# Optimization experiments

Hardware: AMD Instinct MI355X
Metric: run time of the kernel (lower is better)

## Reference

```python
import jax, jax.numpy as jnp
import numpy as np

NODE_DIM = 128
DEPTH = 4
N_NODES = 10000
N_EDGES = 320000


def setup_inputs() -> dict:
    key = jax.random.key(0)
    ks = jax.random.split(key, 12)
    s = 0.05
    D = NODE_DIM
    inp = {
        'h': jax.random.normal(ks[0], (N_NODES, D), jnp.float32),
        'x': jax.random.normal(ks[1], (N_NODES, 3), jnp.float32),
        'edges': jax.random.randint(ks[2], (2, N_EDGES), 0, N_NODES, jnp.int32),
        # edge_mlp: Linear(2D+1 -> D), SiLU, Linear(D -> D), SiLU  (per layer)
        'edge_w1': jax.random.normal(ks[3], (DEPTH, 2 * D + 1, D), jnp.float32) * s,
        'edge_b1': jnp.zeros((DEPTH, D), jnp.float32),
        'edge_w2': jax.random.normal(ks[4], (DEPTH, D, D), jnp.float32) * s,
        'edge_b2': jnp.zeros((DEPTH, D), jnp.float32),
        # node_mlp: Linear(2D -> D), SiLU, Linear(D -> D)  (per layer)
        'node_w1': jax.random.normal(ks[5], (DEPTH, 2 * D, D), jnp.float32) * s,
        'node_b1': jnp.zeros((DEPTH, D), jnp.float32),
        'node_w2': jax.random.normal(ks[6], (DEPTH, D, D), jnp.float32) * s,
        'node_b2': jnp.zeros((DEPTH, D), jnp.float32),
        # coord_mlp (only used by last layer, update_coords=True):
        # Linear(D -> D), SiLU, Linear(D -> 1, bias=False)
        'coord_w1': jax.random.normal(ks[7], (D, D), jnp.float32) * s,
        'coord_b1': jnp.zeros((D,), jnp.float32),
        'coord_w2': jax.random.normal(ks[8], (D, 1), jnp.float32) * s,
    }
    return inp


def reference(h, x, edges, edge_w1, edge_b1, edge_w2, edge_b2,
              node_w1, node_b1, node_w2, node_b2,
              coord_w1, coord_b1, coord_w2):
    silu = jax.nn.silu
    row, col = edges[0], edges[1]
    n = h.shape[0]
    for i in range(DEPTH):
        # coord2radial
        coord_diff = x[row] - x[col]                       # [E, 3]
        radial = jnp.sum(coord_diff * coord_diff, axis=-1, keepdims=True)  # [E, 1]
        # edge_model: m_ij = edge_mlp([h_i, h_j, radial])
        feat = jnp.concatenate([h[row], h[col], radial], axis=-1)  # [E, 2D+1]
        m = silu(feat @ edge_w1[i] + edge_b1[i])
        m = silu(m @ edge_w2[i] + edge_b2[i])              # [E, D]
        # coord_model (only last layer, coords_agg='mean')
        if i == DEPTH - 1:
            w = silu(m @ coord_w1 + coord_b1) @ coord_w2   # [E, 1]
            trans = coord_diff * w                          # [E, 3]
            agg = jax.ops.segment_sum(trans, row, num_segments=n)
            cnt = jax.ops.segment_sum(jnp.ones((row.shape[0], 1), trans.dtype),
                                      row, num_segments=n)
            x = x + agg / jnp.maximum(cnt, 1.0)
        # node_model: h = h + node_mlp([h, sum_j m_ij])  (residual=True)
        magg = jax.ops.segment_sum(m, row, num_segments=n)  # [N, D]
        hin = jnp.concatenate([h, magg], axis=-1)           # [N, 2D]
        out = silu(hin @ node_w1[i] + node_b1[i]) @ node_w2[i] + node_b2[i]
        h = h + out
    return h, x
```

## Files before the change

### kernel.cpp

```cpp
#include <hip/hip_runtime.h>

#define NND 10000
#define NE  320000
#define DD  128
#define NDEPTH 4
#define TE  64

typedef __attribute__((ext_vector_type(8))) short s8b;
typedef __attribute__((ext_vector_type(4))) float f4;
typedef unsigned short u16;
typedef unsigned int   u32;

__device__ __forceinline__ u16 f2b(float f) {
    u32 u = __builtin_bit_cast(u32, f);
    u32 r = (u + 0x7fffu + ((u >> 16) & 1u)) >> 16;
    return (u16)r;
}

__device__ __forceinline__ float b2f(u16 b) {
    u32 u = (u32)b << 16;
    return __builtin_bit_cast(float, u);
}

__device__ __forceinline__ void bpair(u32 v, float& lo, float& hi) {
    lo = __builtin_bit_cast(float, v << 16);
    hi = __builtin_bit_cast(float, v & 0xffff0000u);
}

__device__ __forceinline__ u32 cvt_pk(float lo, float hi) {
    u32 r;
    asm("v_cvt_pk_bf16_f32 %0, %1, %2" : "=v"(r) : "v"(lo), "v"(hi));
    return r;
}

__device__ __forceinline__ u16 f2b1(float v) {
    return (u16)cvt_pk(v, v);
}

__device__ __forceinline__ float silu_f(float v) {
    return v * __builtin_amdgcn_rcpf(1.0f + __expf(-v));
}

__device__ __forceinline__ s8b frag_a(const u16* rowp, int g) {
    union { s8b v; uint2 u2[2]; } r;
    r.u2[0] = *(const uint2*)(rowp + 4 * g);
    r.u2[1] = *(const uint2*)(rowp + 16 + 4 * g);
    return r.v;
}

__device__ __forceinline__ f4 mfma16(s8b a, s8b b, f4 c) {
    return __builtin_amdgcn_mfma_f32_16x16x32_bf16(a, b, c, 0, 0, 0);
}

__global__ __launch_bounds__(256) void egnn_pack(
    const float* __restrict__ ew1, const float* __restrict__ ew2,
    const float* __restrict__ nw1, const float* __restrict__ nw2,
    const float* __restrict__ cw1, u16* __restrict__ pw)
{
    int t = blockIdx.x * 256 + threadIdx.x;
    if (t >= 25 * 16384) return;
    int mat = t >> 14;
    int r   = t & 16383;
    int kt  = r >> 12;
    int nt  = (r >> 9) & 7;
    int lane= (r >> 3) & 63;
    int j   = r & 7;
    int g = lane >> 4, l15 = lane & 15;
    int k = kt * 32 + ((j < 4) ? (4 * g + j) : (16 + 4 * g + (j - 4)));
    int n = nt * 16 + l15;
    float v;
    if (mat < 24) {
        int layer = mat / 6, tp = mat % 6;
        switch (tp) {
            case 0: v = ew1[((size_t)layer * 257 + k) * DD + n]; break;
            case 1: v = ew1[((size_t)layer * 257 + 128 + k) * DD + n]; break;
            case 2: v = ew2[((size_t)layer * 128 + k) * DD + n]; break;
            case 3: v = nw1[((size_t)layer * 256 + k) * DD + n]; break;
            case 4: v = nw1[((size_t)layer * 256 + 128 + k) * DD + n]; break;
            default: v = nw2[((size_t)layer * 128 + k) * DD + n]; break;
        }
    } else {
        v = cw1[(size_t)k * DD + n];
    }
    pw[t] = f2b(v);
}

__global__ __launch_bounds__(256) void egnn_init(
    const float* __restrict__ h, u16* __restrict__ hb)
{
    int i = blockIdx.x * 256 + threadIdx.x;
    size_t base = (size_t)i * 4;
    if (base >= (size_t)NND * DD) return;
    float4 v = *(const float4*)(h + base);
    union { u16 s[4]; uint2 u; } t2;
    t2.s[0] = f2b(v.x); t2.s[1] = f2b(v.y); t2.s[2] = f2b(v.z); t2.s[3] = f2b(v.w);
    *(uint2*)(hb + base) = t2.u;
}

__global__ __launch_bounds__(256) void egnn_count(
    const int* __restrict__ edges, int* __restrict__ cnts)
{
    int e = blockIdx.x * 256 + threadIdx.x;
    if (e < NE) atomicAdd(&cnts[edges[e]], 1);
}

__global__ __launch_bounds__(1024) void egnn_scan(
    const int* __restrict__ cnts, int* __restrict__ off, int* __restrict__ cursor)
{
    __shared__ int part[1024];
    const int t = threadIdx.x;
    const int base = t * 10;
    int s = 0;
    #pragma unroll
    for (int j = 0; j < 10; ++j) {
        int i = base + j;
        s += (i < NND) ? cnts[i] : 0;
    }
    part[t] = s;
    __syncthreads();
    for (int d = 1; d < 1024; d <<= 1) {
        int v = (t >= d) ? part[t - d] : 0;
        __syncthreads();
        part[t] += v;
        __syncthreads();
    }
    int run = (t == 0) ? 0 : part[t - 1];
    #pragma unroll
    for (int j = 0; j < 10; ++j) {
        int i = base + j;
        if (i <= NND) { off[i] = run; cursor[i] = run; }
        if (i < NND) run += cnts[i];
    }
}

__global__ __launch_bounds__(256) void egnn_scatter(
    const int* __restrict__ edges, int* __restrict__ cursor,
    int* __restrict__ rows, int* __restrict__ cols)
{
    int e = blockIdx.x * 256 + threadIdx.x;
    if (e >= NE) return;
    int r = edges[e];
    int p = atomicAdd(&cursor[r], 1);
    rows[p] = r;
    cols[p] = edges[NE + e];
}

__global__ __launch_bounds__(256) void egnn_pre0(
    const u16* __restrict__ hb, const u16* __restrict__ pw,
    const float* __restrict__ eb1,
    float* __restrict__ Pb, u16* __restrict__ Qb)
{
    __shared__ __attribute__((aligned(16))) u16 tH[64][136];
    const int tid = threadIdx.x;
    const int n0  = blockIdx.x * 64;

    #pragma unroll
    for (int it = 0; it < 4; ++it) {
        int idx = tid + it * 256;
        int el = idx >> 4, part = idx & 15;
        int node = n0 + el;
        if (node < NND) {
            *(uint4*)&tH[el][part * 8] = *(const uint4*)(hb + (size_t)node * DD + part * 8);
        } else {
            uint4 z = {0u, 0u, 0u, 0u};
            *(uint4*)&tH[el][part * 8] = z;
        }
    }
    __syncthreads();

    const int wv = tid >> 6, lane = tid & 63;
    const int g = lane >> 4, l15 = lane & 15;
    const int wrow = wv * 16;

    f4 accP[8], accQ[8];
    #pragma unroll
    for (int nt = 0; nt < 8; ++nt) { accP[nt] = f4{0.f,0.f,0.f,0.f}; accQ[nt] = f4{0.f,0.f,0.f,0.f}; }
    const u16* pwa = pw;
    const u16* pwb = pw + 16384;
    #pragma unroll
    for (int kt = 0; kt < 4; ++kt) {
        s8b a = frag_a(&tH[wrow + l15][kt * 32], g);
        const u16* ba = pwa + (size_t)kt * 4096 + lane * 8;
        const u16* bb = pwb + (size_t)kt * 4096 + lane * 8;
        #pragma unroll
        for (int nt = 0; nt < 8; ++nt) {
            accP[nt] = mfma16(a, *(const s8b*)(ba + nt * 512), accP[nt]);
            accQ[nt] = mfma16(a, *(const s8b*)(bb + nt * 512), accQ[nt]);
        }
    }
    #pragma unroll
    for (int nt = 0; nt < 8; ++nt) {
        int n = nt * 16 + l15;
        float bb = eb1[n];
        #pragma unroll
        for (int r = 0; r < 4; ++r) {
            int node = n0 + wrow + g * 4 + r;
            if (node < NND) {
                Pb[(size_t)node * DD + n] = accP[nt][r] + bb;
                Qb[(size_t)node * DD + n] = f2b1(accQ[nt][r]);
            }
        }
    }
}

__global__ __launch_bounds__(256, 6) void egnn_edge(
    const float* __restrict__ Pb, const u16* __restrict__ Qb,
    const float* __restrict__ xin,
    const int* __restrict__ rows, const int* __restrict__ cols,
    const u16* __restrict__ pw,
    const float* __restrict__ ew1,
    const float* __restrict__ eb2, const float* __restrict__ cb1,
    const float* __restrict__ cw2,
    float* __restrict__ magg, float* __restrict__ aggx,
    int layer, int last)
{
    __shared__ __attribute__((aligned(16))) u16 tA[TE][136];
    __shared__ float rad[TE];
    __shared__ float cdf[TE][3];
    __shared__ int   ridx[TE];
    __shared__ int   cidx[TE];
    __shared__ unsigned char segflag[TE + 1];

    const int tid = threadIdx.x;
    const int nblk = NE / TE;
    const int bid  = blockIdx.x;
    const int blk  = (bid & 7) * (nblk >> 3) + (bid >> 3);
    const int p0   = blk * TE;

    if (tid < TE) {
        int p = p0 + tid;
        int r = rows[p];
        int c = cols[p];
        ridx[tid] = r; cidx[tid] = c;
        float d0 = xin[r * 3 + 0] - xin[c * 3 + 0];
        float d1 = xin[r * 3 + 1] - xin[c * 3 + 1];
        float d2 = xin[r * 3 + 2] - xin[c * 3 + 2];
        rad[tid] = d0 * d0 + d1 * d1 + d2 * d2;
        cdf[tid][0] = d0; cdf[tid][1] = d1; cdf[tid][2] = d2;
    }
    __syncthreads();

    if (tid < TE) {
        segflag[tid] = (tid == 0) || (ridx[tid] != ridx[tid - 1]);
        if (tid == 0) segflag[TE] = 1;
    }

    {
        const int cg = tid & 15;
        const int rg = tid >> 4;
        const float* wrp = ew1 + ((size_t)layer * 257 + 256) * DD + cg * 8;
        float4 w0 = *(const float4*)(wrp);
        float4 w4 = *(const float4*)(wrp + 4);
        #pragma unroll
        for (int k = 0; k < 4; ++k) {
            int row = rg + 16 * k;
            int rn = ridx[row], cn = cidx[row];
            float rd = rad[row];
            const float* pp = Pb + (size_t)rn * DD + cg * 8;
            float4 pa = *(const float4*)(pp);
            float4 pc = *(const float4*)(pp + 4);
            uint4 qv = *(const uint4*)(Qb + (size_t)cn * DD + cg * 8);
            float q0, q1, q2, q3, q4, q5, q6, q7;
            bpair(qv.x, q0, q1);
            bpair(qv.y, q2, q3);
            bpair(qv.z, q4, q5);
            bpair(qv.w, q6, q7);
            float v0 = silu_f(pa.x + q0 + rd * w0.x);
            float v1 = silu_f(pa.y + q1 + rd * w0.y);
            float v2 = silu_f(pa.z + q2 + rd * w0.z);
            float v3 = silu_f(pa.w + q3 + rd * w0.w);
            float v4 = silu_f(pc.x + q4 + rd * w4.x);
            float v5 = silu_f(pc.y + q5 + rd * w4.y);
            float v6 = silu_f(pc.z + q6 + rd * w4.z);
            float v7 = silu_f(pc.w + q7 + rd * w4.w);
            union { u32 w[4]; uint4 u; } cv;
            cv.w[0] = cvt_pk(v0, v1);
            cv.w[1] = cvt_pk(v2, v3);
            cv.w[2] = cvt_pk(v4, v5);
            cv.w[3] = cvt_pk(v6, v7);
            *(uint4*)&tA[row][cg * 8] = cv.u;
        }
    }
    __syncthreads();

    const int wv = tid >> 6, lane = tid & 63;
    const int g = lane >> 4, l15 = lane & 15;
    const int wrow = wv * 16;

    f4 acc2[8];
    #pragma unroll
    for (int nt = 0; nt < 8; ++nt) acc2[nt] = f4{0.f, 0.f, 0.f, 0.f};
    const u16* pw2 = pw + (size_t)(layer * 6 + 2) * 16384;
    #pragma unroll
    for (int kt = 0; kt < 4; ++kt) {
        s8b a = frag_a(&tA[wrow + l15][kt * 32], g);
        const u16* pb = pw2 + (size_t)kt * 4096 + lane * 8;
        #pragma unroll
        for (int nt = 0; nt < 8; ++nt) {
            s8b b = *(const s8b*)(pb + nt * 512);
            acc2[nt] = mfma16(a, b, acc2[nt]);
        }
    }
    {
        const float* b2 = eb2 + (size_t)layer * DD;
        #pragma unroll
        for (int nt = 0; nt < 8; ++nt) {
            int n = nt * 16 + l15;
            float bb = b2[n];
            #pragma unroll
            for (int r = 0; r < 4; ++r) {
                int er = wrow + g * 4 + r;
                float v = silu_f(acc2[nt][r] + bb);
                tA[er][n] = f2b1(v);
            }
        }
    }
    __syncthreads();

    if (tid < 128) {
        int col = tid;
        float s = 0.f;
        for (int row = 0; row < TE; ++row) {
            s += b2f(tA[row][col]);
            if (segflag[row + 1] || row == TE - 1) {
                atomicAdd(&magg[(size_t)ridx[row] * DD + col], s);
                s = 0.f;
            }
        }
    }

    if (last) {
        f4 acc3[8];
        #pragma unroll
        for (int nt = 0; nt < 8; ++nt) acc3[nt] = f4{0.f, 0.f, 0.f, 0.f};
        const u16* pwc = pw + (size_t)24 * 16384;
        #pragma unroll
        for (int kt = 0; kt < 4; ++kt) {
            s8b a = frag_a(&tA[wrow + l15][kt * 32], g);
            const u16* pb = pwc + (size_t)kt * 4096 + lane * 8;
            #pragma unroll
            for (int nt = 0; nt < 8; ++nt) {
                s8b b = *(const s8b*)(pb + nt * 512);
                acc3[nt] = mfma16(a, b, acc3[nt]);
            }
        }
        float p[4];
        #pragma unroll
        for (int r = 0; r < 4; ++r) p[r] = 0.f;
        #pragma unroll
        for (int nt = 0; nt < 8; ++nt) {
            int n = nt * 16 + l15;
            float bb = cb1[n], w2 = cw2[n];
            #pragma unroll
            for (int r = 0; r < 4; ++r)
                p[r] += silu_f(acc3[nt][r] + bb) * w2;
        }
        #pragma unroll
        for (int off = 1; off < 16; off <<= 1) {
            #pragma unroll
            for (int r = 0; r < 4; ++r)
                p[r] += __shfl_xor(p[r], off);
        }
        if (l15 == 0) {
            #pragma unroll
            for (int r = 0; r < 4; ++r) {
                int er = wrow + 4 * g + r;
                int rn = ridx[er];
                float w = p[r];
                atomicAdd(&aggx[rn * 3 + 0], cdf[er][0] * w);
                atomicAdd(&aggx[rn * 3 + 1], cdf[er][1] * w);
                atomicAdd(&aggx[rn * 3 + 2], cdf[er][2] * w);
            }
        }
    }
}

__global__ __launch_bounds__(256) void egnn_node(
    const u16* __restrict__ hb, const float* __restrict__ resid,
    const float* __restrict__ magg, const u16* __restrict__ pw,
    const float* __restrict__ nb1, const float* __restrict__ nb2,
    const float* __restrict__ eb1,
    float* __restrict__ out_h, u16* __restrict__ hb_out,
    float* __restrict__ Pb, u16* __restrict__ Qb,
    int layer, int last)
{
    __shared__ __attribute__((aligned(16))) u16 tH[64][136];
    __shared__ __attribute__((aligned(16))) u16 tM[64][136];
    const int tid = threadIdx.x;
    const int n0  = blockIdx.x * 64;

    #pragma unroll
    for (int it = 0; it < 4; ++it) {
        int idx = tid + it * 256;
        int el = idx >> 4, part = idx & 15;
        int node = n0 + el;
        if (node < NND) {
            *(uint4*)&tH[el][part * 8] = *(const uint4*)(hb + (size_t)node * DD + part * 8);
            const float* ms = magg + (size_t)node * DD + part * 8;
            float4 m0 = *(const float4*)(ms);
            float4 m1 = *(const float4*)(ms + 4);
            union { u32 w[4]; uint4 u; } cv;
            cv.w[0] = cvt_pk(m0.x, m0.y);
            cv.w[1] = cvt_pk(m0.z, m0.w);
            cv.w[2] = cvt_pk(m1.x, m1.y);
            cv.w[3] = cvt_pk(m1.z, m1.w);
            *(uint4*)&tM[el][part * 8] = cv.u;
        } else {
            uint4 z = {0u, 0u, 0u, 0u};
            *(uint4*)&tH[el][part * 8] = z;
            *(uint4*)&tM[el][part * 8] = z;
        }
    }
    __syncthreads();

    const int wv = tid >> 6, lane = tid & 63;
    const int g = lane >> 4, l15 = lane & 15;
    const int wrow = wv * 16;

    f4 acc[8];
    #pragma unroll
    for (int nt = 0; nt < 8; ++nt) acc[nt] = f4{0.f, 0.f, 0.f, 0.f};
    const u16* pn1a = pw + (size_t)(layer * 6 + 3) * 16384;
    const u16* pn1b = pw + (size_t)(layer * 6 + 4) * 16384;
    #pragma unroll
    for (int kt = 0; kt < 8; ++kt) {
        const u16 (*tile)[136] = (kt < 4) ? tH : tM;
        const int k0 = (kt & 3) * 32;
        s8b a = frag_a(&tile[wrow + l15][k0], g);
        const u16* pb = ((kt < 4) ? pn1a : pn1b) + (size_t)(kt & 3) * 4096 + lane * 8;
        #pragma unroll
        for (int nt = 0; nt < 8; ++nt) {
            s8b b = *(const s8b*)(pb + nt * 512);
            acc[nt] = mfma16(a, b, acc[nt]);
        }
    }
    {
        const float* b1 = nb1 + (size_t)layer * DD;
        #pragma unroll
        for (int nt = 0; nt < 8; ++nt) {
            int n = nt * 16 + l15;
            float bb = b1[n];
            #pragma unroll
            for (int r = 0; r < 4; ++r) {
                int er = wrow + g * 4 + r;
                tM[er][n] = f2b1(silu_f(acc[nt][r] + bb));
            }
        }
    }
    __syncthreads();

    f4 acc2[8];
    #pragma unroll
    for (int nt = 0; nt < 8; ++nt) acc2[nt] = f4{0.f, 0.f, 0.f, 0.f};
    const u16* pn2 = pw + (size_t)(layer * 6 + 5) * 16384;
    #pragma unroll
    for (int kt = 0; kt < 4; ++kt) {
        s8b a = frag_a(&tM[wrow + l15][kt * 32], g);
        const u16* pb = pn2 + (size_t)kt * 4096 + lane * 8;
        #pragma unroll
        for (int nt = 0; nt < 8; ++nt) {
            s8b b = *(const s8b*)(pb + nt * 512);
            acc2[nt] = mfma16(a, b, acc2[nt]);
        }
    }
    {
        const float* b2 = nb2 + (size_t)layer * DD;
        #pragma unroll
        for (int nt = 0; nt < 8; ++nt) {
            int n = nt * 16 + l15;
            float bb = b2[n];
            #pragma unroll
            for (int r = 0; r < 4; ++r) {
                int er = wrow + g * 4 + r;
                int node = n0 + er;
                if (node < NND) {
                    float v = acc2[nt][r] + bb + resid[(size_t)node * DD + n];
                    out_h[(size_t)node * DD + n] = v;
                    if (!last) {
                        u16 hv = f2b1(v);
                        hb_out[(size_t)node * DD + n] = hv;
                        tH[er][n] = hv;
                    }
                } else if (!last) {
                    tH[er][n] = 0;
                }
            }
        }
    }

    if (!last) {
        __syncthreads();
        f4 accP[8], accQ[8];
        #pragma unroll
        for (int nt = 0; nt < 8; ++nt) { accP[nt] = f4{0.f,0.f,0.f,0.f}; accQ[nt] = f4{0.f,0.f,0.f,0.f}; }
        const u16* pwa = pw + (size_t)((layer + 1) * 6 + 0) * 16384;
        const u16* pwb = pw + (size_t)((layer + 1) * 6 + 1) * 16384;
        #pragma unroll
        for (int kt = 0; kt < 4; ++kt) {
            s8b a = frag_a(&tH[wrow + l15][kt * 32], g);
            const u16* ba = pwa + (size_t)kt * 4096 + lane * 8;
            const u16* bb = pwb + (size_t)kt * 4096 + lane * 8;
            #pragma unroll
            for (int nt = 0; nt < 8; ++nt) {
                accP[nt] = mfma16(a, *(const s8b*)(ba + nt * 512), accP[nt]);
                accQ[nt] = mfma16(a, *(const s8b*)(bb + nt * 512), accQ[nt]);
            }
        }
        #pragma unroll
        for (int nt = 0; nt < 8; ++nt) {
            int n = nt * 16 + l15;
            float bb = eb1[(size_t)(layer + 1) * DD + n];
            #pragma unroll
            for (int r = 0; r < 4; ++r) {
                int node = n0 + wrow + g * 4 + r;
                if (node < NND) {
                    Pb[(size_t)node * DD + n] = accP[nt][r] + bb;
                    Qb[(size_t)node * DD + n] = f2b1(accQ[nt][r]);
                }
            }
        }
    }
}

__global__ __launch_bounds__(256) void egnn_coord_out(
    const float* __restrict__ xin, const float* __restrict__ aggx,
    const int* __restrict__ off, float* __restrict__ out_x)
{
    int i = blockIdx.x * 256 + threadIdx.x;
    if (i >= NND) return;
    float c = (float)(off[i + 1] - off[i]);
    float inv = 1.0f / fmaxf(c, 1.0f);
    out_x[i * 3 + 0] = xin[i * 3 + 0] + aggx[i * 3 + 0] * inv;
    out_x[i * 3 + 1] = xin[i * 3 + 1] + aggx[i * 3 + 1] * inv;
    out_x[i * 3 + 2] = xin[i * 3 + 2] + aggx[i * 3 + 2] * inv;
}

extern "C" void kernel_launch(void* const* d_in, const int* in_sizes, int n_in,
                              void* d_out, int out_size, void* d_ws, size_t ws_size,
                              hipStream_t stream) {
    const float* h   = (const float*)d_in[0];
    const float* x   = (const float*)d_in[1];
    const int*  edges= (const int*)d_in[2];
    const float* ew1 = (const float*)d_in[3];
    const float* eb1 = (const float*)d_in[4];
    const float* ew2 = (const float*)d_in[5];
    const float* eb2 = (const float*)d_in[6];
    const float* nw1 = (const float*)d_in[7];
    const float* nb1 = (const float*)d_in[8];
    const float* nw2 = (const float*)d_in[9];
    const float* nb2 = (const float*)d_in[10];
    const float* cw1 = (const float*)d_in[11];
    const float* cb1 = (const float*)d_in[12];
    const float* cw2 = (const float*)d_in[13];

    char* ws = (char*)d_ws;
    u16*   hb   = (u16*)  (ws);
    u16*   pw   = (u16*)  (ws + 2560000);
    int*   cnts = (int*)  (ws + 3379200);
    int*   off  = (int*)  (ws + 3419216);
    int*   curs = (int*)  (ws + 3459232);
    int*   rows = (int*)  (ws + 3499248);
    int*   cols = (int*)  (ws + 4779248);
    float* aggx = (float*)(ws + 6059248);
    float* Pb   = (float*)(ws + 6179312);
    u16*   Qb   = (u16*)  (ws + 11299312);
    float* magg = (float*)(ws + 13859312);

    float* out_h = (float*)d_out;
    float* out_x = out_h + (size_t)NND * DD;

    egnn_pack<<<1600, 256, 0, stream>>>(ew1, ew2, nw1, nw2, cw1, pw);
    egnn_init<<<1250, 256, 0, stream>>>(h, hb);
    hipMemsetAsync(aggx, 0, 120064, stream);
    hipMemsetAsync(cnts, 0, 40016, stream);

    egnn_count<<<1250, 256, 0, stream>>>(edges, cnts);
    egnn_scan<<<1, 1024, 0, stream>>>(cnts, off, curs);
    egnn_scatter<<<1250, 256, 0, stream>>>(edges, curs, rows, cols);
    egnn_pre0<<<(NND + 63) / 64, 256, 0, stream>>>(hb, pw, eb1, Pb, Qb);

    for (int i = 0; i < NDEPTH; ++i) {
        int last = (i == NDEPTH - 1);
        hipMemsetAsync(magg, 0, (size_t)NND * DD * 4, stream);
        egnn_edge<<<NE / TE, 256, 0, stream>>>(Pb, Qb, x, rows, cols, pw,
                                               ew1, eb2, cb1, cw2,
                                               magg, aggx, i, last);
        const float* resid = (i == 0) ? h : (const float*)out_h;
        egnn_node<<<(NND + 63) / 64, 256, 0, stream>>>(hb, resid, magg, pw, nb1, nb2, eb1,
                                                       out_h, hb, Pb, Qb, i, last);
    }
    egnn_coord_out<<<40, 256, 0, stream>>>(x, aggx, off, out_x);
}
```

Measured before the change: 500.2 us.

## Build first-layer MFMA A-fragments in registers instead of staging through LDS

Each lane now gathers the P/Q rows and the radial weights for its own MFMA row, applies SiLU, and packs the bf16 A-fragments straight into registers. This drops the shared-memory write of the first-layer activations, the fragment reads and a __syncthreads. The cost is more register pressure from 8 float4 and 8 uint2 live loads, so launch bounds are lowered from 6 to 4 blocks per SM. Gathers also become narrower and less coalesced (16-byte P chunks and 8-byte Q chunks per lane, rows scattered across lanes).

```diff
diff --git a/kernel.cpp b/kernel.cpp
--- a/kernel.cpp
+++ b/kernel.cpp
@@ -203,7 +203,7 @@
     }
 }
 
-__global__ __launch_bounds__(256, 6) void egnn_edge(
+__global__ __launch_bounds__(256, 4) void egnn_edge(
     const float* __restrict__ Pb, const u16* __restrict__ Qb,
     const float* __restrict__ xin,
     const int* __restrict__ rows, const int* __restrict__ cols,
@@ -237,6 +237,7 @@
         float d2 = xin[r * 3 + 2] - xin[c * 3 + 2];
         rad[tid] = d0 * d0 + d1 * d1 + d2 * d2;
         cdf[tid][0] = d0; cdf[tid][1] = d1; cdf[tid][2] = d2;
+        segflag[tid] = 0;
     }
     __syncthreads();
 
@@ -245,60 +246,67 @@
         if (tid == 0) segflag[TE] = 1;
     }
 
-    {
-        const int cg = tid & 15;
-        const int rg = tid >> 4;
-        const float* wrp = ew1 + ((size_t)layer * 257 + 256) * DD + cg * 8;
-        float4 w0 = *(const float4*)(wrp);
-        float4 w4 = *(const float4*)(wrp + 4);
-        #pragma unroll
-        for (int k = 0; k < 4; ++k) {
-            int row = rg + 16 * k;
-            int rn = ridx[row], cn = cidx[row];
-            float rd = rad[row];
-            const float* pp = Pb + (size_t)rn * DD + cg * 8;
-            float4 pa = *(const float4*)(pp);
-            float4 pc = *(const float4*)(pp + 4);
-            uint4 qv = *(const uint4*)(Qb + (size_t)cn * DD + cg * 8);
-            float q0, q1, q2, q3, q4, q5, q6, q7;
-            bpair(qv.x, q0, q1);
-            bpair(qv.y, q2, q3);
-            bpair(qv.z, q4, q5);
-            bpair(qv.w, q6, q7);
-            float v0 = silu_f(pa.x + q0 + rd * w0.x);
-            float v1 = silu_f(pa.y + q1 + rd * w0.y);
-            float v2 = silu_f(pa.z + q2 + rd * w0.z);
-            float v3 = silu_f(pa.w + q3 + rd * w0.w);
-            float v4 = silu_f(pc.x + q4 + rd * w4.x);
-            float v5 = silu_f(pc.y + q5 + rd * w4.y);
-            float v6 = silu_f(pc.z + q6 + rd * w4.z);
-            float v7 = silu_f(pc.w + q7 + rd * w4.w);
-            union { u32 w[4]; uint4 u; } cv;
-            cv.w[0] = cvt_pk(v0, v1);
-            cv.w[1] = cvt_pk(v2, v3);
-            cv.w[2] = cvt_pk(v4, v5);
-            cv.w[3] = cvt_pk(v6, v7);
-            *(uint4*)&tA[row][cg * 8] = cv.u;
-        }
-    }
-    __syncthreads();
-
     const int wv = tid >> 6, lane = tid & 63;
     const int g = lane >> 4, l15 = lane & 15;
     const int wrow = wv * 16;
 
+    const int myrow = wrow + l15;
+    const int rn = ridx[myrow];
+    const int cn = cidx[myrow];
+    const float rd = rad[myrow];
+    const float* Pr = Pb + (size_t)rn * DD;
+    const u16*   Qr = Qb + (size_t)cn * DD;
+    const float* Wr = ew1 + ((size_t)layer * 257 + 256) * DD;
+    const int c0 = 4 * g;
+
+    float4 pv[8];
+    uint2  qv[8];
+    #pragma unroll
+    for (int kt = 0; kt < 4; ++kt) {
+        int ca = kt * 32 + c0;
+        pv[2*kt]   = *(const float4*)(Pr + ca);
+        pv[2*kt+1] = *(const float4*)(Pr + ca + 16);
+        qv[2*kt]   = *(const uint2*)(Qr + ca);
+        qv[2*kt+1] = *(const uint2*)(Qr + ca + 16);
+    }
+
+    s8b mfrag[4];
+    #pragma unroll
+    for (int kt = 0; kt < 4; ++kt) {
+        int ca = kt * 32 + c0;
+        float4 wa = *(const float4*)(Wr + ca);
+        float4 wb = *(const float4*)(Wr + ca + 16);
+        float qa0, qa1, qa2, qa3, qb0, qb1, qb2, qb3;
+        bpair(qv[2*kt].x,   qa0, qa1); bpair(qv[2*kt].y,   qa2, qa3);
+        bpair(qv[2*kt+1].x, qb0, qb1); bpair(qv[2*kt+1].y, qb2, qb3);
+        float4 p0 = pv[2*kt], p1 = pv[2*kt+1];
+        float a0 = silu_f(p0.x + qa0 + rd * wa.x);
+        float a1 = silu_f(p0.y + qa1 + rd * wa.y);
+        float a2 = silu_f(p0.z + qa2 + rd * wa.z);
+        float a3 = silu_f(p0.w + qa3 + rd * wa.w);
+        float b0 = silu_f(p1.x + qb0 + rd * wb.x);
+        float b1 = silu_f(p1.y + qb1 + rd * wb.y);
+        float b2 = silu_f(p1.z + qb2 + rd * wb.z);
+        float b3 = silu_f(p1.w + qb3 + rd * wb.w);
+        union { s8b v; u32 w[4]; } fr;
+        fr.w[0] = cvt_pk(a0, a1);
+        fr.w[1] = cvt_pk(a2, a3);
+        fr.w[2] = cvt_pk(b0, b1);
+        fr.w[3] = cvt_pk(b2, b3);
+        mfrag[kt] = fr.v;
+    }
+
     f4 acc2[8];
     #pragma unroll
     for (int nt = 0; nt < 8; ++nt) acc2[nt] = f4{0.f, 0.f, 0.f, 0.f};
     const u16* pw2 = pw + (size_t)(layer * 6 + 2) * 16384;
     #pragma unroll
     for (int kt = 0; kt < 4; ++kt) {
-        s8b a = frag_a(&tA[wrow + l15][kt * 32], g);
         const u16* pb = pw2 + (size_t)kt * 4096 + lane * 8;
         #pragma unroll
         for (int nt = 0; nt < 8; ++nt) {
             s8b b = *(const s8b*)(pb + nt * 512);
-            acc2[nt] = mfma16(a, b, acc2[nt]);
+            acc2[nt] = mfma16(mfrag[kt], b, acc2[nt]);
         }
     }
     {
@@ -365,11 +373,11 @@
             #pragma unroll
             for (int r = 0; r < 4; ++r) {
                 int er = wrow + 4 * g + r;
-                int rn = ridx[er];
+                int rn2 = ridx[er];
                 float w = p[r];
-                atomicAdd(&aggx[rn * 3 + 0], cdf[er][0] * w);
-                atomicAdd(&aggx[rn * 3 + 1], cdf[er][1] * w);
-                atomicAdd(&aggx[rn * 3 + 2], cdf[er][2] * w);
+                atomicAdd(&aggx[rn2 * 3 + 0], cdf[er][0] * w);
+                atomicAdd(&aggx[rn2 * 3 + 1], cdf[er][1] * w);
+                atomicAdd(&aggx[rn2 * 3 + 2], cdf[er][2] * w);
             }
         }
     }
```

Result: slower. 578.0 us (+15.6%).

## Partition edge kernel by destination-node groups to replace global atomics with local reduction

Applied to the files above, without the earlier changes.

The edge kernel now assigns each block a group of 4 destination nodes and walks their CSR-sorted edge range in 64-edge tiles. It accumulates messages and coordinate updates in shared memory and writes bf16 aggregates once per node. This removes the per-layer memset of the fp32 aggregate buffer and the global atomicAdd traffic, and lets the node kernel read bf16 directly. In exchange, load balance now depends on node degree, partially filled tiles waste MFMA work, and only 2500 blocks each run a serial tile loop.

```diff
diff --git a/kernel.cpp b/kernel.cpp
--- a/kernel.cpp
+++ b/kernel.cpp
@@ -5,6 +5,7 @@
 #define DD  128
 #define NDEPTH 4
 #define TE  64
+#define GN  4
 
 typedef __attribute__((ext_vector_type(8))) short s8b;
 typedef __attribute__((ext_vector_type(4))) float f4;
@@ -207,177 +208,193 @@
     const float* __restrict__ Pb, const u16* __restrict__ Qb,
     const float* __restrict__ xin,
     const int* __restrict__ rows, const int* __restrict__ cols,
+    const int* __restrict__ off,
     const u16* __restrict__ pw,
     const float* __restrict__ ew1,
     const float* __restrict__ eb2, const float* __restrict__ cb1,
     const float* __restrict__ cw2,
-    float* __restrict__ magg, float* __restrict__ aggx,
+    u16* __restrict__ maggb, float* __restrict__ aggx,
     int layer, int last)
 {
     __shared__ __attribute__((aligned(16))) u16 tA[TE][136];
+    __shared__ __attribute__((aligned(16))) float Pg[GN][DD];
+    __shared__ float wrL[DD];
+    __shared__ float maccL[GN][DD];
+    __shared__ float aggL[GN][3];
     __shared__ float rad[TE];
     __shared__ float cdf[TE][3];
     __shared__ int   ridx[TE];
     __shared__ int   cidx[TE];
-    __shared__ unsigned char segflag[TE + 1];
-
-    const int tid = threadIdx.x;
-    const int nblk = NE / TE;
-    const int bid  = blockIdx.x;
-    const int blk  = (bid & 7) * (nblk >> 3) + (bid >> 3);
-    const int p0   = blk * TE;
-
-    if (tid < TE) {
-        int p = p0 + tid;
-        int r = rows[p];
-        int c = cols[p];
-        ridx[tid] = r; cidx[tid] = c;
-        float d0 = xin[r * 3 + 0] - xin[c * 3 + 0];
-        float d1 = xin[r * 3 + 1] - xin[c * 3 + 1];
-        float d2 = xin[r * 3 + 2] - xin[c * 3 + 2];
-        rad[tid] = d0 * d0 + d1 * d1 + d2 * d2;
-        cdf[tid][0] = d0; cdf[tid][1] = d1; cdf[tid][2] = d2;
-    }
-    __syncthreads();
-
-    if (tid < TE) {
-        segflag[tid] = (tid == 0) || (ridx[tid] != ridx[tid - 1]);
-        if (tid == 0) segflag[TE] = 1;
-    }
-
-    {
-        const int cg = tid & 15;
-        const int rg = tid >> 4;
-        const float* wrp = ew1 + ((size_t)layer * 257 + 256) * DD + cg * 8;
-        float4 w0 = *(const float4*)(wrp);
-        float4 w4 = *(const float4*)(wrp + 4);
-        #pragma unroll
-        for (int k = 0; k < 4; ++k) {
-            int row = rg + 16 * k;
-            int rn = ridx[row], cn = cidx[row];
-            float rd = rad[row];
-            const float* pp = Pb + (size_t)rn * DD + cg * 8;
-            float4 pa = *(const float4*)(pp);
-            float4 pc = *(const float4*)(pp + 4);
-            uint4 qv = *(const uint4*)(Qb + (size_t)cn * DD + cg * 8);
-            float q0, q1, q2, q3, q4, q5, q6, q7;
-            bpair(qv.x, q0, q1);
-            bpair(qv.y, q2, q3);
-            bpair(qv.z, q4, q5);
-            bpair(qv.w, q6, q7);
-            float v0 = silu_f(pa.x + q0 + rd * w0.x);
-            float v1 = silu_f(pa.y + q1 + rd * w0.y);
-            float v2 = silu_f(pa.z + q2 + rd * w0.z);
-            float v3 = silu_f(pa.w + q3 + rd * w0.w);
-            float v4 = silu_f(pc.x + q4 + rd * w4.x);
-            float v5 = silu_f(pc.y + q5 + rd * w4.y);
-            float v6 = silu_f(pc.z + q6 + rd * w4.z);
-            float v7 = silu_f(pc.w + q7 + rd * w4.w);
-            union { u32 w[4]; uint4 u; } cv;
-            cv.w[0] = cvt_pk(v0, v1);
-            cv.w[1] = cvt_pk(v2, v3);
-            cv.w[2] = cvt_pk(v4, v5);
-            cv.w[3] = cvt_pk(v6, v7);
-            *(uint4*)&tA[row][cg * 8] = cv.u;
-        }
-    }
-    __syncthreads();
+    __shared__ unsigned char segflag[TE];
+
+    const int tid  = threadIdx.x;
+    const int base = blockIdx.x * GN;
+    const int e0 = off[base], e1 = off[base + GN];
+
+    ((float2*)&Pg[0][0])[tid] = ((const float2*)(Pb + (size_t)base * DD))[tid];
+    if (tid < 64)
+        ((float2*)wrL)[tid] = ((const float2*)(ew1 + ((size_t)layer * 257 + 256) * DD))[tid];
+    ((float2*)&maccL[0][0])[tid] = float2{0.f, 0.f};
+    if (tid < GN * 3) ((float*)aggL)[tid] = 0.f;
 
     const int wv = tid >> 6, lane = tid & 63;
     const int g = lane >> 4, l15 = lane & 15;
     const int wrow = wv * 16;
-
-    f4 acc2[8];
-    #pragma unroll
-    for (int nt = 0; nt < 8; ++nt) acc2[nt] = f4{0.f, 0.f, 0.f, 0.f};
+    const int cg = tid & 15, rg = tid >> 4;
     const u16* pw2 = pw + (size_t)(layer * 6 + 2) * 16384;
-    #pragma unroll
-    for (int kt = 0; kt < 4; ++kt) {
-        s8b a = frag_a(&tA[wrow + l15][kt * 32], g);
-        const u16* pb = pw2 + (size_t)kt * 4096 + lane * 8;
-        #pragma unroll
-        for (int nt = 0; nt < 8; ++nt) {
-            s8b b = *(const s8b*)(pb + nt * 512);
-            acc2[nt] = mfma16(a, b, acc2[nt]);
-        }
-    }
-    {
-        const float* b2 = eb2 + (size_t)layer * DD;
+    const u16* pwc = pw + (size_t)24 * 16384;
+    const float* b2p = eb2 + (size_t)layer * DD;
+
+    for (int t0 = e0; t0 < e1; t0 += TE) {
+        const int nv = min(TE, e1 - t0);
+        __syncthreads();
+        if (tid < TE) {
+            int p = t0 + (tid < nv ? tid : 0);
+            int r = rows[p], c = cols[p];
+            ridx[tid] = r; cidx[tid] = c;
+            float d0 = xin[r * 3 + 0] - xin[c * 3 + 0];
+            float d1 = xin[r * 3 + 1] - xin[c * 3 + 1];
+            float d2 = xin[r * 3 + 2] - xin[c * 3 + 2];
+            rad[tid] = d0 * d0 + d1 * d1 + d2 * d2;
+            cdf[tid][0] = d0; cdf[tid][1] = d1; cdf[tid][2] = d2;
+        }
+        __syncthreads();
+        if (tid < TE)
+            segflag[tid] = (tid == 0) || (ridx[tid] != ridx[tid - 1]);
+
+        {
+            float4 w0 = *(const float4*)&wrL[cg * 8];
+            float4 w4 = *(const float4*)&wrL[cg * 8 + 4];
+            #pragma unroll
+            for (int k = 0; k < 4; ++k) {
+                int row = rg + 16 * k;
+                int ln = ridx[row] - base;
+                float rd = rad[row];
+                int cn = cidx[row];
+                float4 pa = *(const float4*)&Pg[ln][cg * 8];
+                float4 pc = *(const float4*)&Pg[ln][cg * 8 + 4];
+                uint4 qv = *(const uint4*)(Qb + (size_t)cn * DD + cg * 8);
+                float q0, q1, q2, q3, q4, q5, q6, q7;
+                bpair(qv.x, q0, q1);
+                bpair(qv.y, q2, q3);
+                bpair(qv.z, q4, q5);
+                bpair(qv.w, q6, q7);
+                float v0 = silu_f(pa.x + q0 + rd * w0.x);
+                float v1 = silu_f(pa.y + q1 + rd * w0.y);
+                float v2 = silu_f(pa.z + q2 + rd * w0.z);
+                float v3 = silu_f(pa.w + q3 + rd * w0.w);
+                float v4 = silu_f(pc.x + q4 + rd * w4.x);
+                float v5 = silu_f(pc.y + q5 + rd * w4.y);
+                float v6 = silu_f(pc.z + q6 + rd * w4.z);
+                float v7 = silu_f(pc.w + q7 + rd * w4.w);
+                union { u32 w[4]; uint4 u; } cv;
+                cv.w[0] = cvt_pk(v0, v1);
+                cv.w[1] = cvt_pk(v2, v3);
+                cv.w[2] = cvt_pk(v4, v5);
+                cv.w[3] = cvt_pk(v6, v7);
+                *(uint4*)&tA[row][cg * 8] = cv.u;
+            }
+        }
+        __syncthreads();
+
+        f4 acc2[8];
+        #pragma unroll
+        for (int nt = 0; nt < 8; ++nt) acc2[nt] = f4{0.f, 0.f, 0.f, 0.f};
+        #pragma unroll
+        for (int kt = 0; kt < 4; ++kt) {
+            s8b a = frag_a(&tA[wrow + l15][kt * 32], g);
+            const u16* pb = pw2 + (size_t)kt * 4096 + lane * 8;
+            #pragma unroll
+            for (int nt = 0; nt < 8; ++nt) {
+                s8b b = *(const s8b*)(pb + nt * 512);
+                acc2[nt] = mfma16(a, b, acc2[nt]);
+            }
+        }
         #pragma unroll
         for (int nt = 0; nt < 8; ++nt) {
             int n = nt * 16 + l15;
-            float bb = b2[n];
+            float bb = b2p[n];
             #pragma unroll
             for (int r = 0; r < 4; ++r) {
                 int er = wrow + g * 4 + r;
-                float v = silu_f(acc2[nt][r] + bb);
-                tA[er][n] = f2b1(v);
+                tA[er][n] = f2b1(silu_f(acc2[nt][r] + bb));
+            }
+        }
+        __syncthreads();
+
+        if (tid < 128) {
+            int col = tid;
+            float s = 0.f;
+            for (int row = 0; row < nv; ++row) {
+                s += b2f(tA[row][col]);
+                if (row == nv - 1 || segflag[row + 1]) {
+                    maccL[ridx[row] - base][col] += s;
+                    s = 0.f;
+                }
+            }
+        }
+
+        if (last) {
+            f4 acc3[8];
+            #pragma unroll
+            for (int nt = 0; nt < 8; ++nt) acc3[nt] = f4{0.f, 0.f, 0.f, 0.f};
+            #pragma unroll
+            for (int kt = 0; kt < 4; ++kt) {
+                s8b a = frag_a(&tA[wrow + l15][kt * 32], g);
+                const u16* pb = pwc + (size_t)kt * 4096 + lane * 8;
+                #pragma unroll
+                for (int nt = 0; nt < 8; ++nt) {
+                    s8b b = *(const s8b*)(pb + nt * 512);
+                    acc3[nt] = mfma16(a, b, acc3[nt]);
+                }
+            }
+            float p[4];
+            #pragma unroll
+            for (int r = 0; r < 4; ++r) p[r] = 0.f;
+            #pragma unroll
+            for (int nt = 0; nt < 8; ++nt) {
+                int n = nt * 16 + l15;
+                float bb = cb1[n], w2 = cw2[n];
+                #pragma unroll
+                for (int r = 0; r < 4; ++r)
+                    p[r] += silu_f(acc3[nt][r] + bb) * w2;
+            }
+            #pragma unroll
+            for (int o = 1; o < 16; o <<= 1) {
+                #pragma unroll
+                for (int r = 0; r < 4; ++r)
+                    p[r] += __shfl_xor(p[r], o);
+            }
+            if (l15 == 0) {
+                #pragma unroll
+                for (int r = 0; r < 4; ++r) {
+                    int er = wrow + 4 * g + r;
+                    if (er < nv) {
+                        int ln = ridx[er] - base;
+                        float w = p[r];
+                        atomicAdd(&aggL[ln][0], cdf[er][0] * w);
+                        atomicAdd(&aggL[ln][1], cdf[er][1] * w);
+                        atomicAdd(&aggL[ln][2], cdf[er][2] * w);
+                    }
+                }
             }
         }
     }
     __syncthreads();
 
-    if (tid < 128) {
-        int col = tid;
-        float s = 0.f;
-        for (int row = 0; row < TE; ++row) {
-            s += b2f(tA[row][col]);
-            if (segflag[row + 1] || row == TE - 1) {
-                atomicAdd(&magg[(size_t)ridx[row] * DD + col], s);
-                s = 0.f;
-            }
-        }
-    }
-
-    if (last) {
-        f4 acc3[8];
-        #pragma unroll
-        for (int nt = 0; nt < 8; ++nt) acc3[nt] = f4{0.f, 0.f, 0.f, 0.f};
-        const u16* pwc = pw + (size_t)24 * 16384;
-        #pragma unroll
-        for (int kt = 0; kt < 4; ++kt) {
-            s8b a = frag_a(&tA[wrow + l15][kt * 32], g);
-            const u16* pb = pwc + (size_t)kt * 4096 + lane * 8;
-            #pragma unroll
-            for (int nt = 0; nt < 8; ++nt) {
-                s8b b = *(const s8b*)(pb + nt * 512);
-                acc3[nt] = mfma16(a, b, acc3[nt]);
-            }
-        }
-        float p[4];
-        #pragma unroll
-        for (int r = 0; r < 4; ++r) p[r] = 0.f;
-        #pragma unroll
-        for (int nt = 0; nt < 8; ++nt) {
-            int n = nt * 16 + l15;
-            float bb = cb1[n], w2 = cw2[n];
-            #pragma unroll
-            for (int r = 0; r < 4; ++r)
-                p[r] += silu_f(acc3[nt][r] + bb) * w2;
-        }
-        #pragma unroll
-        for (int off = 1; off < 16; off <<= 1) {
-            #pragma unroll
-            for (int r = 0; r < 4; ++r)
-                p[r] += __shfl_xor(p[r], off);
-        }
-        if (l15 == 0) {
-            #pragma unroll
-            for (int r = 0; r < 4; ++r) {
-                int er = wrow + 4 * g + r;
-                int rn = ridx[er];
-                float w = p[r];
-                atomicAdd(&aggx[rn * 3 + 0], cdf[er][0] * w);
-                atomicAdd(&aggx[rn * 3 + 1], cdf[er][1] * w);
-                atomicAdd(&aggx[rn * 3 + 2], cdf[er][2] * w);
-            }
-        }
+    {
+        int l = tid >> 6, cp = tid & 63;
+        u32 w = cvt_pk(maccL[l][cp * 2], maccL[l][cp * 2 + 1]);
+        *(u32*)(maggb + (size_t)(base + l) * DD + cp * 2) = w;
+    }
+    if (last && tid < GN * 3) {
+        aggx[base * 3 + tid] = ((const float*)aggL)[tid];
     }
 }
 
 __global__ __launch_bounds__(256) void egnn_node(
     const u16* __restrict__ hb, const float* __restrict__ resid,
-    const float* __restrict__ magg, const u16* __restrict__ pw,
+    const u16* __restrict__ maggb, const u16* __restrict__ pw,
     const float* __restrict__ nb1, const float* __restrict__ nb2,
     const float* __restrict__ eb1,
     float* __restrict__ out_h, u16* __restrict__ hb_out,
@@ -396,15 +413,7 @@
         int node = n0 + el;
         if (node < NND) {
             *(uint4*)&tH[el][part * 8] = *(const uint4*)(hb + (size_t)node * DD + part * 8);
-            const float* ms = magg + (size_t)node * DD + part * 8;
-            float4 m0 = *(const float4*)(ms);
-            float4 m1 = *(const float4*)(ms + 4);
-            union { u32 w[4]; uint4 u; } cv;
-            cv.w[0] = cvt_pk(m0.x, m0.y);
-            cv.w[1] = cvt_pk(m0.z, m0.w);
-            cv.w[2] = cvt_pk(m1.x, m1.y);
-            cv.w[3] = cvt_pk(m1.z, m1.w);
-            *(uint4*)&tM[el][part * 8] = cv.u;
+            *(uint4*)&tM[el][part * 8] = *(const uint4*)(maggb + (size_t)node * DD + part * 8);
         } else {
             uint4 z = {0u, 0u, 0u, 0u};
             *(uint4*)&tH[el][part * 8] = z;
@@ -564,14 +573,13 @@
     float* aggx = (float*)(ws + 6059248);
     float* Pb   = (float*)(ws + 6179312);
     u16*   Qb   = (u16*)  (ws + 11299312);
-    float* magg = (float*)(ws + 13859312);
+    u16*   maggb= (u16*)  (ws + 13859312);
 
     float* out_h = (float*)d_out;
     float* out_x = out_h + (size_t)NND * DD;
 
     egnn_pack<<<1600, 256, 0, stream>>>(ew1, ew2, nw1, nw2, cw1, pw);
     egnn_init<<<1250, 256, 0, stream>>>(h, hb);
-    hipMemsetAsync(aggx, 0, 120064, stream);
     hipMemsetAsync(cnts, 0, 40016, stream);
 
     egnn_count<<<1250, 256, 0, stream>>>(edges, cnts);
@@ -581,12 +589,11 @@
 
     for (int i = 0; i < NDEPTH; ++i) {
         int last = (i == NDEPTH - 1);
-        hipMemsetAsync(magg, 0, (size_t)NND * DD * 4, stream);
-        egnn_edge<<<NE / TE, 256, 0, stream>>>(Pb, Qb, x, rows, cols, pw,
-                                               ew1, eb2, cb1, cw2,
-                                               magg, aggx, i, last);
+        egnn_edge<<<NND / GN, 256, 0, stream>>>(Pb, Qb, x, rows, cols, off, pw,
+                                                ew1, eb2, cb1, cw2,
+                                                maggb, aggx, i, last);
         const float* resid = (i == 0) ? h : (const float*)out_h;
-        egnn_node<<<(NND + 63) / 64, 256, 0, stream>>>(hb, resid, magg, pw, nb1, nb2, eb1,
+        egnn_node<<<(NND + 63) / 64, 256, 0, stream>>>(hb, resid, maggb, pw, nb1, nb2, eb1,
                                                        out_h, hb, Pb, Qb, i, last);
     }
     egnn_coord_out<<<40, 256, 0, stream>>>(x, aggx, off, out_x);
```

After: 927.7 us. 85.5% more time.
